# Performance work log

Hardware: AMD Instinct MI355X
Metric: run time of the kernel (lower is better)

Reference implementation:

```python
import jax, jax.numpy as jnp
import numpy as np

EMBED = 1024
HEADS = 16
HEAD_DIM = EMBED // HEADS
MASKED_BIAS = -10000.0


def setup_inputs() -> dict:
    key = jax.random.key(0)
    k1, k2, k3 = jax.random.split(key, 3)
    hidden_states = jax.random.normal(k1, (4, 2048, EMBED), dtype=jnp.float32)
    c_attn_w = jax.random.normal(k2, (EMBED, 3 * EMBED), dtype=jnp.float32) * 0.02
    c_attn_b = jnp.zeros((3 * EMBED,), dtype=jnp.float32)
    c_proj_w = jax.random.normal(k3, (EMBED, EMBED), dtype=jnp.float32) * 0.02
    c_proj_b = jnp.zeros((EMBED,), dtype=jnp.float32)
    return {
        "hidden_states": hidden_states,
        "c_attn_w": c_attn_w,
        "c_attn_b": c_attn_b,
        "c_proj_w": c_proj_w,
        "c_proj_b": c_proj_b,
    }


def reference(hidden_states, c_attn_w, c_attn_b, c_proj_w, c_proj_b):
    B, S, E = hidden_states.shape
    # QKV projection (Conv1D == x @ W + b)
    qkv = hidden_states @ c_attn_w + c_attn_b  # [B,S,3E]
    q, k, v = jnp.split(qkv, 3, axis=-1)
    def split_heads(t):
        return t.reshape(B, S, HEADS, HEAD_DIM).transpose(0, 2, 1, 3)  # [B,H,S,D]
    q, k, v = split_heads(q), split_heads(k), split_heads(v)
    # scaled attention scores
    scores = jnp.einsum("bhqd,bhkd->bhqk", q, k) / jnp.float32(HEAD_DIM) ** 0.5
    causal = jnp.tril(jnp.ones((S, S), dtype=bool))
    scores = jnp.where(causal[None, None], scores, jnp.float32(MASKED_BIAS))
    attn_weights = jax.nn.softmax(scores, axis=-1)
    attn_out = jnp.einsum("bhqk,bhkd->bhqd", attn_weights, v)
    attn_out = attn_out.transpose(0, 2, 1, 3).reshape(B, S, E)
    out = attn_out @ c_proj_w + c_proj_b
    return out
```

## Files before the change

kernel.cpp:

```cpp
#include <hip/hip_runtime.h>
#include <hip/hip_bf16.h>

#define EMB 1024
#define SEQ 2048
#define ATT_SCALE 0.18033688011112042f

typedef __bf16 bf16x8 __attribute__((ext_vector_type(8)));
typedef float f32x4 __attribute__((ext_vector_type(4)));
typedef float f32x16 __attribute__((ext_vector_type(16)));

__device__ __forceinline__ unsigned short f2bf(float f) {
    union { float f; unsigned int u; } v; v.f = f;
    unsigned int r = (v.u + 0x7FFFu + ((v.u >> 16) & 1u)) >> 16;
    return (unsigned short)r;
}

__device__ __forceinline__ void async_load16(const void* g, void* l) {
    __builtin_amdgcn_global_load_lds(
        (const __attribute__((address_space(1))) unsigned int*)g,
        (__attribute__((address_space(3))) unsigned int*)l, 16, 0, 0);
}

__global__ void cvt_bf16(const float4* __restrict__ in, ushort4* __restrict__ out, int n4) {
    int i = blockIdx.x * blockDim.x + threadIdx.x;
    int stride = gridDim.x * blockDim.x;
    for (; i < n4; i += stride) {
        float4 v = in[i];
        ushort4 o;
        o.x = f2bf(v.x); o.y = f2bf(v.y); o.z = f2bf(v.z); o.w = f2bf(v.w);
        out[i] = o;
    }
}

__global__ void transpose_cvt(const float* __restrict__ in, unsigned short* __restrict__ out,
                              int R, int C) {
    __shared__ float tile[32][33];
    int bx = blockIdx.x * 32;
    int by = blockIdx.y * 32;
    int tx = threadIdx.x & 31;
    int ty = threadIdx.x >> 5;
    #pragma unroll
    for (int i = 0; i < 32; i += 8)
        tile[ty + i][tx] = in[(size_t)(by + ty + i) * C + bx + tx];
    __syncthreads();
    #pragma unroll
    for (int i = 0; i < 32; i += 8)
        out[(size_t)(bx + ty + i) * R + by + tx] = f2bf(tile[tx][ty + i]);
}

#define BM 128
#define BN 128
#define BK 64

template<bool OUT_BF16>
__global__ __launch_bounds__(256, 2)
void gemm_bf16(const unsigned short* __restrict__ A,
               const unsigned short* __restrict__ Bt,
               const float* __restrict__ bias,
               void* __restrict__ Cout,
               int M, int N, int K) {
    __shared__ unsigned short As[BM * 64];
    __shared__ unsigned short Bs[BN * 64];
    const int tid = threadIdx.x;
    const int m0 = blockIdx.y * BM;
    const int n0 = blockIdx.x * BN;
    const int lane = tid & 63;
    const int wave = tid >> 6;
    const int wm = (wave & 1) * 64;
    const int wn = (wave >> 1) * 64;
    const int lm = lane & 15;
    const int quad = lane >> 4;
    const int r8 = lane >> 3;
    const int pc = lane & 7;

    f32x4 acc[4][4] = {};

    for (int k0 = 0; k0 < K; k0 += BK) {
        __syncthreads();
        #pragma unroll
        for (int i = 0; i < 4; i++) {
            int r = wave * 32 + i * 8 + r8;
            int lc = pc ^ (r & 7);
            async_load16(&A[(size_t)(m0 + r) * K + k0 + lc * 8], &As[(wave * 32 + i * 8) * 64]);
            async_load16(&Bt[(size_t)(n0 + r) * K + k0 + lc * 8], &Bs[(wave * 32 + i * 8) * 64]);
        }
        __syncthreads();
        #pragma unroll
        for (int kk = 0; kk < 2; kk++) {
            bf16x8 af[4], bfr[4];
            #pragma unroll
            for (int t = 0; t < 4; t++) {
                int phys = ((kk * 4 + quad) ^ (lm & 7)) << 3;
                af[t]  = *(const bf16x8*)&As[(wm + t * 16 + lm) * 64 + phys];
                bfr[t] = *(const bf16x8*)&Bs[(wn + t * 16 + lm) * 64 + phys];
            }
            #pragma unroll
            for (int mt = 0; mt < 4; mt++)
                #pragma unroll
                for (int nt = 0; nt < 4; nt++)
                    acc[mt][nt] = __builtin_amdgcn_mfma_f32_16x16x32_bf16(
                        af[mt], bfr[nt], acc[mt][nt], 0, 0, 0);
        }
    }
    #pragma unroll
    for (int mt = 0; mt < 4; mt++) {
        #pragma unroll
        for (int nt = 0; nt < 4; nt++) {
            int col = n0 + wn + nt * 16 + lm;
            float bv = bias[col];
            #pragma unroll
            for (int r = 0; r < 4; r++) {
                int row = m0 + wm + mt * 16 + quad * 4 + r;
                float val = acc[mt][nt][r] + bv;
                if (OUT_BF16)
                    ((unsigned short*)Cout)[(size_t)row * N + col] = f2bf(val);
                else
                    ((float*)Cout)[(size_t)row * N + col] = val;
            }
        }
    }
}

__global__ void transpose_v(const unsigned short* __restrict__ qkv,
                            unsigned short* __restrict__ vt) {
    __shared__ unsigned short T[64 * 72];
    const int tid = threadIdx.x;
    const int sb = blockIdx.x;
    const int bh = blockIdx.y;
    const int b = bh >> 4;
    const int h = bh & 15;
    const unsigned short* src = qkv + (size_t)(b * SEQ + sb * 64) * 3072 + 2 * EMB + h * 64;
    #pragma unroll
    for (int i = 0; i < 2; i++) {
        int c = tid + 256 * i;
        int row = c >> 3;
        int col = (c & 7) * 8;
        *(uint4*)&T[row * 72 + col] = *(const uint4*)&src[(size_t)row * 3072 + col];
    }
    __syncthreads();
    unsigned short* dst = vt + (size_t)bh * 64 * SEQ + sb * 64;
    #pragma unroll
    for (int i = 0; i < 2; i++) {
        int c = tid + 256 * i;
        int dr = c >> 3;
        int sc = (c & 7) * 8;
        unsigned short tmp[8];
        #pragma unroll
        for (int j = 0; j < 8; j++) tmp[j] = T[(sc + j) * 72 + dr];
        *(uint4*)&dst[(size_t)dr * SEQ + sc] = *(uint4*)tmp;
    }
}

__global__ __launch_bounds__(256, 3)
void attention(const unsigned short* __restrict__ qkv,
               const unsigned short* __restrict__ vt,
               unsigned short* __restrict__ outb) {
    __shared__ unsigned short smem[128 * 72];
    unsigned short* Ks = smem;
    unsigned short* Vs = smem + 64 * 72;
    const int tid = threadIdx.x;
    const int lane = tid & 63;
    const int wave = tid >> 6;
    const int l31 = lane & 31;
    const int half = lane >> 5;
    const int bh = blockIdx.y;
    const int b = bh >> 4;
    const int h = bh & 15;
    const int srow0 = tid >> 3;
    const int sch  = (tid & 7) * 8;

    for (int ph = 0; ph < 2; ph++) {
        const int qt = ph ? (15 - blockIdx.x) : blockIdx.x;
        const int qs = qt * 128 + wave * 32 + l31;
        const size_t qgrow = (size_t)b * SEQ + qs;

        bf16x8 qf[4];
        #pragma unroll
        for (int dt = 0; dt < 4; dt++)
            qf[dt] = *(const bf16x8*)&qkv[qgrow * 3072 + h * 64 + dt * 16 + half * 8];

        f32x16 o[2] = {};
        float m_prev = -1e30f, lsum = 0.f;

        const int nkb = 2 * qt + 2;
        const int qmax_w = qt * 128 + wave * 32 + 31;

        uint4 kreg[2], vreg[2];
        #pragma unroll
        for (int i = 0; i < 2; i++) {
            int row = srow0 + 32 * i;
            kreg[i] = *(const uint4*)&qkv[(size_t)(b * SEQ + row) * 3072 + EMB + h * 64 + sch];
            vreg[i] = *(const uint4*)&vt[(size_t)(bh * 64 + row) * SEQ + sch];
        }

        for (int kb = 0; kb < nkb; kb++) {
            __syncthreads();
            #pragma unroll
            for (int i = 0; i < 2; i++) {
                int row = srow0 + 32 * i;
                *(uint4*)&Ks[row * 72 + sch] = kreg[i];
                *(uint4*)&Vs[row * 72 + sch] = vreg[i];
            }
            __syncthreads();
            if (kb + 1 < nkb) {
                #pragma unroll
                for (int i = 0; i < 2; i++) {
                    int row = srow0 + 32 * i;
                    kreg[i] = *(const uint4*)&qkv[(size_t)(b * SEQ + (kb + 1) * 64 + row) * 3072 + EMB + h * 64 + sch];
                    vreg[i] = *(const uint4*)&vt[(size_t)(bh * 64 + row) * SEQ + (kb + 1) * 64 + sch];
                }
            }

            if (kb * 64 > qmax_w) continue;

            f32x16 st[2] = {};
            #pragma unroll
            for (int dt = 0; dt < 4; dt++) {
                #pragma unroll
                for (int ct = 0; ct < 2; ct++) {
                    bf16x8 kf = *(const bf16x8*)&Ks[(ct * 32 + l31) * 72 + dt * 16 + half * 8];
                    st[ct] = __builtin_amdgcn_mfma_f32_32x32x16_bf16(kf, qf[dt], st[ct], 0, 0, 0);
                }
            }

            if (kb * 64 + 63 > qt * 128 + wave * 32) {
                #pragma unroll
                for (int ct = 0; ct < 2; ct++)
                    #pragma unroll
                    for (int r = 0; r < 16; r++) {
                        int cg = kb * 64 + ct * 32 + (r & 3) + 8 * (r >> 2) + 4 * half;
                        if (cg > qs) st[ct][r] = -1e9f;
                    }
            }

            float mx = -1e30f;
            #pragma unroll
            for (int r = 0; r < 16; r++) mx = fmaxf(mx, fmaxf(st[0][r], st[1][r]));
            mx = fmaxf(mx, __shfl_xor(mx, 32, 64));
            float m_new = fmaxf(m_prev, mx);
            float alpha = exp2f((m_prev - m_new) * ATT_SCALE);
            float nmc = -m_new * ATT_SCALE;
            float sum = 0.f;
            #pragma unroll
            for (int r = 0; r < 16; r++) {
                st[0][r] = exp2f(__builtin_fmaf(st[0][r], ATT_SCALE, nmc));
                st[1][r] = exp2f(__builtin_fmaf(st[1][r], ATT_SCALE, nmc));
                sum += st[0][r] + st[1][r];
            }
            sum += __shfl_xor(sum, 32, 64);
            lsum = lsum * alpha + sum;
            m_prev = m_new;
            #pragma unroll
            for (int r = 0; r < 16; r++) { o[0][r] *= alpha; o[1][r] *= alpha; }

            unsigned int pk[2][8];
            #pragma unroll
            for (int t = 0; t < 2; t++)
                #pragma unroll
                for (int i = 0; i < 8; i++) {
                    __hip_bfloat162 pb = __float22bfloat162_rn(float2{st[t][2 * i], st[t][2 * i + 1]});
                    union { __hip_bfloat162 b; unsigned int u; } cv; cv.b = pb;
                    pk[t][i] = cv.u;
                }

            #pragma unroll
            for (int kt = 0; kt < 4; kt++) {
                const int t = kt >> 1, e = kt & 1;
                unsigned int own0 = half ? pk[t][4 * e + 2] : pk[t][4 * e + 0];
                unsigned int own1 = half ? pk[t][4 * e + 3] : pk[t][4 * e + 1];
                unsigned int snd0 = half ? pk[t][4 * e + 0] : pk[t][4 * e + 2];
                unsigned int snd1 = half ? pk[t][4 * e + 1] : pk[t][4 * e + 3];
                unsigned int rcv0 = (unsigned int)__shfl_xor((int)snd0, 32, 64);
                unsigned int rcv1 = (unsigned int)__shfl_xor((int)snd1, 32, 64);
                union { uint4 u; bf16x8 v; } pf;
                pf.u.x = half ? rcv0 : own0;
                pf.u.y = half ? rcv1 : own1;
                pf.u.z = half ? own0 : rcv0;
                pf.u.w = half ? own1 : rcv1;
                #pragma unroll
                for (int dt = 0; dt < 2; dt++) {
                    bf16x8 vf = *(const bf16x8*)&Vs[(dt * 32 + l31) * 72 + kt * 16 + half * 8];
                    o[dt] = __builtin_amdgcn_mfma_f32_32x32x16_bf16(vf, pf.v, o[dt], 0, 0, 0);
                }
            }
        }

        __syncthreads();
        float inv = 1.0f / lsum;
        #pragma unroll
        for (int dt = 0; dt < 2; dt++)
            #pragma unroll
            for (int r = 0; r < 16; r++) {
                int d = dt * 32 + (r & 3) + 8 * (r >> 2) + 4 * half;
                smem[(wave * 32 + l31) * 72 + d] = f2bf(o[dt][r] * inv);
            }
        __syncthreads();
        #pragma unroll
        for (int i = 0; i < 4; i++) {
            int c = tid + 256 * i;
            int row = c >> 3;
            int ch = (c & 7) * 8;
            uint4 v = *(const uint4*)&smem[row * 72 + ch];
            *(uint4*)&outb[(size_t)(b * SEQ + qt * 128 + row) * EMB + h * 64 + ch] = v;
        }
    }
}

extern "C" void kernel_launch(void* const* d_in, const int* in_sizes, int n_in,
                              void* d_out, int out_size, void* d_ws, size_t ws_size,
                              hipStream_t stream) {
    const float* X     = (const float*)d_in[0];
    const float* Wqkv  = (const float*)d_in[1];
    const float* bqkv  = (const float*)d_in[2];
    const float* Wproj = (const float*)d_in[3];
    const float* bproj = (const float*)d_in[4];
    float* out = (float*)d_out;

    char* ws = (char*)d_ws;
    unsigned short* Xb     = (unsigned short*)(ws);
    unsigned short* WqkvT  = (unsigned short*)(ws + 16777216);
    unsigned short* WprojT = (unsigned short*)(ws + 23068672);
    unsigned short* qkvb   = (unsigned short*)(ws + 25165824);
    unsigned short* Vt     = (unsigned short*)(ws + 75497472);
    unsigned short* attnb  = (unsigned short*)(ws + 92274688);

    cvt_bf16<<<2048, 256, 0, stream>>>((const float4*)X, (ushort4*)Xb, (4 * 2048 * 1024) / 4);
    transpose_cvt<<<dim3(3072 / 32, 1024 / 32), 256, 0, stream>>>(Wqkv, WqkvT, 1024, 3072);
    transpose_cvt<<<dim3(1024 / 32, 1024 / 32), 256, 0, stream>>>(Wproj, WprojT, 1024, 1024);
    gemm_bf16<true><<<dim3(3072 / BN, 8192 / BM), 256, 0, stream>>>(
        Xb, WqkvT, bqkv, qkvb, 8192, 3072, 1024);
    transpose_v<<<dim3(32, 64), 256, 0, stream>>>(qkvb, Vt);
    attention<<<dim3(8, 64), 256, 0, stream>>>(qkvb, Vt, attnb);
    gemm_bf16<false><<<dim3(1024 / BN, 8192 / BM), 256, 0, stream>>>(
        attnb, WprojT, bproj, out, 8192, 1024, 1024);
}
```

Baseline: 300.3 us.

## Double-buffer K/V LDS tiles in attention and tree-reduce softmax max/sum

The attention kernel now keeps two K/V LDS buffers selected by the parity of kb. This removes one of the two __syncthreads per key block, and the barrier is placed after the next tile's global loads are issued. The softmax row max and row sum switch from serial chains to tree reductions, which shortens dependency chains. The grid is swapped so blockIdx.x indexes batch-head and blockIdx.y the query tile, which changes block scheduling order. LDS use doubles and occupancy is lowered from 3 to 2 blocks per SM, and an extra barrier is added at the end of each phase to protect the buffer reuse.

New measurement: 311.5 us. 3.7% more time.

```diff
diff --git a/kernel.cpp b/kernel.cpp
--- a/kernel.cpp
+++ b/kernel.cpp
@@ -151,26 +151,24 @@
     }
 }
 
-__global__ __launch_bounds__(256, 3)
+__global__ __launch_bounds__(256, 2)
 void attention(const unsigned short* __restrict__ qkv,
                const unsigned short* __restrict__ vt,
                unsigned short* __restrict__ outb) {
-    __shared__ unsigned short smem[128 * 72];
-    unsigned short* Ks = smem;
-    unsigned short* Vs = smem + 64 * 72;
+    __shared__ unsigned short smem[4 * 64 * 72];
     const int tid = threadIdx.x;
     const int lane = tid & 63;
     const int wave = tid >> 6;
     const int l31 = lane & 31;
     const int half = lane >> 5;
-    const int bh = blockIdx.y;
+    const int bh = blockIdx.x;
     const int b = bh >> 4;
     const int h = bh & 15;
     const int srow0 = tid >> 3;
     const int sch  = (tid & 7) * 8;
 
     for (int ph = 0; ph < 2; ph++) {
-        const int qt = ph ? (15 - blockIdx.x) : blockIdx.x;
+        const int qt = ph ? (15 - (int)blockIdx.y) : (int)blockIdx.y;
         const int qs = qt * 128 + wave * 32 + l31;
         const size_t qgrow = (size_t)b * SEQ + qs;
 
@@ -194,14 +192,14 @@
         }
 
         for (int kb = 0; kb < nkb; kb++) {
-            __syncthreads();
+            unsigned short* Ks = smem + (kb & 1) * 2 * 64 * 72;
+            unsigned short* Vs = Ks + 64 * 72;
             #pragma unroll
             for (int i = 0; i < 2; i++) {
                 int row = srow0 + 32 * i;
                 *(uint4*)&Ks[row * 72 + sch] = kreg[i];
                 *(uint4*)&Vs[row * 72 + sch] = vreg[i];
             }
-            __syncthreads();
             if (kb + 1 < nkb) {
                 #pragma unroll
                 for (int i = 0; i < 2; i++) {
@@ -210,6 +208,7 @@
                     vreg[i] = *(const uint4*)&vt[(size_t)(bh * 64 + row) * SEQ + (kb + 1) * 64 + sch];
                 }
             }
+            __syncthreads();
 
             if (kb * 64 > qmax_w) continue;
 
@@ -233,21 +232,32 @@
                     }
             }
 
-            float mx = -1e30f;
-            #pragma unroll
-            for (int r = 0; r < 16; r++) mx = fmaxf(mx, fmaxf(st[0][r], st[1][r]));
-            mx = fmaxf(mx, __shfl_xor(mx, 32, 64));
+            float tm[8];
+            #pragma unroll
+            for (int r = 0; r < 8; r++)
+                tm[r] = fmaxf(fmaxf(st[0][r], st[1][r]), fmaxf(st[0][r + 8], st[1][r + 8]));
+            #pragma unroll
+            for (int s = 4; s > 0; s >>= 1)
+                #pragma unroll
+                for (int r = 0; r < s; r++) tm[r] = fmaxf(tm[r], tm[r + s]);
+            float mx = fmaxf(tm[0], __shfl_xor(tm[0], 32, 64));
             float m_new = fmaxf(m_prev, mx);
             float alpha = exp2f((m_prev - m_new) * ATT_SCALE);
             float nmc = -m_new * ATT_SCALE;
-            float sum = 0.f;
             #pragma unroll
             for (int r = 0; r < 16; r++) {
                 st[0][r] = exp2f(__builtin_fmaf(st[0][r], ATT_SCALE, nmc));
                 st[1][r] = exp2f(__builtin_fmaf(st[1][r], ATT_SCALE, nmc));
-                sum += st[0][r] + st[1][r];
-            }
-            sum += __shfl_xor(sum, 32, 64);
+            }
+            float ts[8];
+            #pragma unroll
+            for (int r = 0; r < 8; r++)
+                ts[r] = (st[0][r] + st[1][r]) + (st[0][r + 8] + st[1][r + 8]);
+            #pragma unroll
+            for (int s = 4; s > 0; s >>= 1)
+                #pragma unroll
+                for (int r = 0; r < s; r++) ts[r] += ts[r + s];
+            float sum = ts[0] + __shfl_xor(ts[0], 32, 64);
             lsum = lsum * alpha + sum;
             m_prev = m_new;
             #pragma unroll
@@ -303,6 +313,7 @@
             uint4 v = *(const uint4*)&smem[row * 72 + ch];
             *(uint4*)&outb[(size_t)(b * SEQ + qt * 128 + row) * EMB + h * 64 + ch] = v;
         }
+        __syncthreads();
     }
 }
 
@@ -330,7 +341,7 @@
     gemm_bf16<true><<<dim3(3072 / BN, 8192 / BM), 256, 0, stream>>>(
         Xb, WqkvT, bqkv, qkvb, 8192, 3072, 1024);
     transpose_v<<<dim3(32, 64), 256, 0, stream>>>(qkvb, Vt);
-    attention<<<dim3(8, 64), 256, 0, stream>>>(qkvb, Vt, attnb);
+    attention<<<dim3(64, 8), 256, 0, stream>>>(qkvb, Vt, attnb);
     gemm_bf16<false><<<dim3(1024 / BN, 8192 / BM), 256, 0, stream>>>(
         attnb, WprojT, bproj, out, 8192, 1024, 1024);
 }
```
